# Optimization experiments

Measured on AMD Instinct MI355X. Metric: run time of the kernel, lower is better.

Reference implementation:

```python
import jax, jax.numpy as jnp
import numpy as np

B, C, D = 4096, 1000, 3072


def setup_inputs() -> dict:
    key = jax.random.key(0)
    k1, k2, k3, k4 = jax.random.split(key, 4)
    scale = 1.0
    return {
        "z": jax.random.normal(k1, (B, D), dtype=jnp.float32),
        "sldj": jax.random.normal(k2, (B,), dtype=jnp.float32),
        "labels": jax.random.randint(k3, (B,), 0, C),
        "beta": jnp.ones((), dtype=jnp.float32),
        "means": jax.random.normal(k4, (C, D), dtype=jnp.float32) * scale,
    }


def reference(z, sldj, labels, beta, means):
    # dists[i,j] = -0.5 * ||z_i - mu_j||^2, via a^2 + b^2 - 2ab GEMM trick
    z2 = jnp.sum(z * z, axis=1, keepdims=True)          # [B,1]
    m2 = jnp.sum(means * means, axis=1)[None, :]        # [1,C]
    cross = jnp.einsum('bd,cd->bc', z, means)           # [B,C] GEMM
    dists = -0.5 * (z2 + m2 - 2.0 * cross)              # [B,C]

    log_pz = jax.nn.logsumexp(dists, axis=1)            # [B]
    # cross_entropy(dists, labels) = mean(logsumexp - dists[i, y_i])
    picked = jnp.take_along_axis(dists, labels[:, None], axis=1)[:, 0]
    loss_cls = jnp.mean(log_pz - picked)
    loss_gen = -jnp.mean(log_pz + sldj) / z.shape[1]
    total = loss_gen + beta * loss_cls
    return total, loss_gen, loss_cls
```

## Files before the change

### kernel.cpp

```cpp
#include <hip/hip_runtime.h>
#include <hip/hip_bf16.h>
#include <cstdint>
#include <cstddef>

#define NB 4096
#define NC 1000
#define NCP 1024
#define ND 3072
#define NSL 4
#define KSL (ND / NSL)
#define BM 128
#define BN 128
#define BK 32
#define NT (KSL / BK)
#define ABUF (BM * BK)
#define BBUF (BN * BK)

typedef __attribute__((ext_vector_type(8))) __bf16 bf16x8;
typedef __attribute__((ext_vector_type(4))) float f32x4;
typedef __attribute__((ext_vector_type(4))) unsigned short u16x4;
typedef __attribute__((ext_vector_type(4))) _Float16 f16x4;
typedef unsigned short u16;

__device__ __forceinline__ u16 f2bf_rne(float x) {
    uint32_t u = __float_as_uint(x);
    uint32_t r = (u + 0x7fffu + ((u >> 16) & 1u)) >> 16;
    return (u16)r;
}

__global__ __launch_bounds__(256) void convert_all_kernel(
        const float* __restrict__ z, const float* __restrict__ means,
        u16* __restrict__ zb, u16* __restrict__ mb,
        float* __restrict__ z2, float* __restrict__ m2) {
    const int bidx = blockIdx.x;
    const int tid = threadIdx.x;
    const float* src;
    u16* dst;
    float* sq;
    bool pad = false;
    if (bidx < NB) {
        src = z + (size_t)bidx * ND;
        dst = zb + (size_t)bidx * ND;
        sq = z2 + bidx;
    } else {
        const int mr = bidx - NB;
        dst = mb + (size_t)mr * ND;
        sq = m2 + mr;
        src = means + (size_t)mr * ND;
        pad = (mr >= NC);
    }
    if (!pad) {
        const float4* s = (const float4*)src;
        float acc = 0.f;
#pragma unroll
        for (int i = 0; i < 3; ++i) {
            const int idx = tid + i * 256;
            float4 v = s[idx];
            acc = fmaf(v.x, v.x, acc);
            acc = fmaf(v.y, v.y, acc);
            acc = fmaf(v.z, v.z, acc);
            acc = fmaf(v.w, v.w, acc);
            u16x4 o;
            o.x = f2bf_rne(v.x); o.y = f2bf_rne(v.y);
            o.z = f2bf_rne(v.z); o.w = f2bf_rne(v.w);
            *(u16x4*)(dst + idx * 4) = o;
        }
#pragma unroll
        for (int off = 32; off > 0; off >>= 1) acc += __shfl_xor(acc, off, 64);
        __shared__ float ssum[4];
        const int wid = tid >> 6, lane = tid & 63;
        if (lane == 0) ssum[wid] = acc;
        __syncthreads();
        if (tid == 0) sq[0] = ssum[0] + ssum[1] + ssum[2] + ssum[3];
    } else {
        u16x4 z4 = (u16x4){0, 0, 0, 0};
#pragma unroll
        for (int i = 0; i < 3; ++i) *(u16x4*)(dst + (tid + i * 256) * 4) = z4;
        if (tid == 0) sq[0] = 1e30f;
    }
}

#define GLOAD_LDS16(gp, lp)                                            \
    __builtin_amdgcn_global_load_lds(                                  \
        (const __attribute__((address_space(1))) void*)(gp),           \
        (__attribute__((address_space(3))) void*)(lp), 16, 0, 0)

__global__ __launch_bounds__(256, 4) void gemm_kernel(
        const u16* __restrict__ zb, const u16* __restrict__ mb,
        _Float16* __restrict__ crossh) {
    __shared__ u16 As[2 * ABUF];
    __shared__ u16 Bs[2 * BBUF];

    const int tid  = threadIdx.x;
    const int wid  = tid >> 6;
    const int lane = tid & 63;
    const int wr   = wid >> 1;
    const int wc   = wid & 1;
    const int lrow = lane & 15;
    const int kgrp = lane >> 4;

    const int bid = blockIdx.x;
    const int w = (bid & 7) * 128 + (bid >> 3);
    const int bcol8 = w & 7;
    const int brow  = ((w >> 3) & 31) * BM;
    const int ksl   = w >> 8;
    const int bcol  = bcol8 * BN;
    const int kbase = ksl * KSL;

    f32x4 acc[4][4];
#pragma unroll
    for (int m = 0; m < 4; ++m)
#pragma unroll
        for (int n = 0; n < 4; ++n) acc[m][n] = (f32x4){0.f, 0.f, 0.f, 0.f};

    const u16* gA[2]; const u16* gB[2];
    u16* lA[2];       u16* lB[2];
#pragma unroll
    for (int g = 0; g < 2; ++g) {
        const int c = g * 256 + tid;
        const int r = c >> 2, p = c & 3, s = p ^ ((r >> 1) & 3);
        gA[g] = zb + (size_t)(brow + r) * ND + kbase + s * 8;
        gB[g] = mb + (size_t)(bcol + r) * ND + kbase + s * 8;
        lA[g] = As + (g * 256 + wid * 64) * 8;
        lB[g] = Bs + (g * 256 + wid * 64) * 8;
    }

#define STAGE(tt) do {                                                   \
        const int bb_ = (tt) & 1;                                        \
        const int ko_ = (tt) * BK;                                       \
        GLOAD_LDS16(gA[0] + ko_, lA[0] + bb_ * ABUF);                    \
        GLOAD_LDS16(gA[1] + ko_, lA[1] + bb_ * ABUF);                    \
        GLOAD_LDS16(gB[0] + ko_, lB[0] + bb_ * BBUF);                    \
        GLOAD_LDS16(gB[1] + ko_, lB[1] + bb_ * BBUF);                    \
    } while (0)

#define COMP(tt) do {                                                    \
        const int cb_ = (tt) & 1;                                        \
        const u16* Ac = As + cb_ * ABUF;                                 \
        const u16* Bc = Bs + cb_ * BBUF;                                 \
        const int pk = kgrp ^ ((lrow >> 1) & 3);                         \
        bf16x8 a0 = *(const bf16x8*)&Ac[(wr * 64 +  0 + lrow) * BK + pk * 8]; \
        bf16x8 a1 = *(const bf16x8*)&Ac[(wr * 64 + 16 + lrow) * BK + pk * 8]; \
        bf16x8 a2 = *(const bf16x8*)&Ac[(wr * 64 + 32 + lrow) * BK + pk * 8]; \
        bf16x8 a3 = *(const bf16x8*)&Ac[(wr * 64 + 48 + lrow) * BK + pk * 8]; \
        _Pragma("unroll")                                                \
        for (int n = 0; n < 4; ++n) {                                    \
            bf16x8 bn = *(const bf16x8*)&Bc[(wc * 64 + n * 16 + lrow) * BK + pk * 8]; \
            acc[0][n] = __builtin_amdgcn_mfma_f32_16x16x32_bf16(a0, bn, acc[0][n], 0, 0, 0); \
            acc[1][n] = __builtin_amdgcn_mfma_f32_16x16x32_bf16(a1, bn, acc[1][n], 0, 0, 0); \
            acc[2][n] = __builtin_amdgcn_mfma_f32_16x16x32_bf16(a2, bn, acc[2][n], 0, 0, 0); \
            acc[3][n] = __builtin_amdgcn_mfma_f32_16x16x32_bf16(a3, bn, acc[3][n], 0, 0, 0); \
        }                                                                \
    } while (0)

    STAGE(0);

    for (int t = 0; t < NT; ++t) {
        asm volatile("s_waitcnt vmcnt(0)" ::: "memory");
        __builtin_amdgcn_s_barrier();
        __builtin_amdgcn_sched_barrier(0);
        if (t + 1 < NT) STAGE(t + 1);
        __builtin_amdgcn_sched_barrier(0);
        COMP(t);
    }

#undef STAGE
#undef COMP

    _Float16* outp = crossh + (size_t)ksl * NB * NCP;
#pragma unroll
    for (int n = 0; n < 4; ++n) {
        const int gcol = bcol + wc * 64 + n * 16 + lrow;
#pragma unroll
        for (int m = 0; m < 4; ++m) {
#pragma unroll
            for (int r = 0; r < 4; ++r) {
                const int grow = brow + wr * 64 + m * 16 + kgrp * 4 + r;
                outp[(size_t)grow * NCP + gcol] = (_Float16)acc[m][n][r];
            }
        }
    }
}

__global__ __launch_bounds__(256) void row_lse_kernel(
        const _Float16* __restrict__ crossh, const float* __restrict__ m2,
        const int* __restrict__ labels, const float* __restrict__ sldj,
        float* __restrict__ outA, float* __restrict__ outB) {
    const int row = blockIdx.x;
    const int tid = threadIdx.x;

    float a0 = 0.f, a1 = 0.f, a2 = 0.f, a3 = 0.f;
#pragma unroll
    for (int s = 0; s < NSL; ++s) {
        f16x4 h = ((const f16x4*)(crossh + ((size_t)s * NB + row) * NCP))[tid];
        a0 += (float)h.x; a1 += (float)h.y; a2 += (float)h.z; a3 += (float)h.w;
    }
    float4 mm = ((const float4*)m2)[tid];
    float4 v;
    v.x = a0 - 0.5f * mm.x;
    v.y = a1 - 0.5f * mm.y;
    v.z = a2 - 0.5f * mm.z;
    v.w = a3 - 0.5f * mm.w;

    float mx = fmaxf(fmaxf(v.x, v.y), fmaxf(v.z, v.w));
#pragma unroll
    for (int off = 32; off > 0; off >>= 1) mx = fmaxf(mx, __shfl_xor(mx, off, 64));
    __shared__ float smax[4], ssum[4];
    const int wid = tid >> 6, lane = tid & 63;
    if (lane == 0) smax[wid] = mx;
    __syncthreads();
    const float bm = fmaxf(fmaxf(smax[0], smax[1]), fmaxf(smax[2], smax[3]));

    float s = expf(v.x - bm) + expf(v.y - bm) + expf(v.z - bm) + expf(v.w - bm);
#pragma unroll
    for (int off = 32; off > 0; off >>= 1) s += __shfl_xor(s, off, 64);
    if (lane == 0) ssum[wid] = s;
    __syncthreads();
    if (tid == 0) {
        const float tot = ssum[0] + ssum[1] + ssum[2] + ssum[3];
        const float lpz = bm + logf(tot);
        const int lab = labels[row];
        float pick = 0.f;
#pragma unroll
        for (int si = 0; si < NSL; ++si)
            pick += (float)crossh[((size_t)si * NB + row) * NCP + lab];
        pick -= 0.5f * m2[lab];
        outA[row] = lpz - pick;
        outB[row] = lpz + sldj[row];
    }
}

__global__ __launch_bounds__(1024) void finalize_kernel(
        const float* __restrict__ a, const float* __restrict__ b,
        const float* __restrict__ z2, const float* __restrict__ beta,
        float* __restrict__ out) {
    __shared__ float sa[1024], sb[1024], sz[1024];
    const int tid = threadIdx.x;
    float va = 0.f, vb = 0.f, vz = 0.f;
    for (int i = tid; i < NB; i += 1024) {
        va += a[i]; vb += b[i]; vz += z2[i];
    }
    sa[tid] = va; sb[tid] = vb; sz[tid] = vz;
    __syncthreads();
    for (int s = 512; s > 0; s >>= 1) {
        if (tid < s) {
            sa[tid] += sa[tid + s];
            sb[tid] += sb[tid + s];
            sz[tid] += sz[tid + s];
        }
        __syncthreads();
    }
    if (tid == 0) {
        const float loss_cls = sa[0] / (float)NB;
        const float mean_lpz_sldj = sb[0] / (float)NB - 0.5f * (sz[0] / (float)NB);
        const float loss_gen = -mean_lpz_sldj / (float)ND;
        const float total = loss_gen + beta[0] * loss_cls;
        out[0] = total;
        out[1] = loss_gen;
        out[2] = loss_cls;
    }
}

extern "C" void kernel_launch(void* const* d_in, const int* in_sizes, int n_in,
                              void* d_out, int out_size, void* d_ws, size_t ws_size,
                              hipStream_t stream) {
    const float* z      = (const float*)d_in[0];
    const float* sldj   = (const float*)d_in[1];
    const int*   labels = (const int*)d_in[2];
    const float* beta   = (const float*)d_in[3];
    const float* means  = (const float*)d_in[4];
    float* out = (float*)d_out;

    char* ws = (char*)d_ws;
    size_t off = 0;
    u16* zb = (u16*)(ws + off);           off += (size_t)NB * ND * 2;
    u16* mb = (u16*)(ws + off);           off += (size_t)NCP * ND * 2;
    float* z2 = (float*)(ws + off);       off += (size_t)NB * 4;
    float* m2 = (float*)(ws + off);       off += (size_t)NCP * 4;
    _Float16* crossh = (_Float16*)(ws + off); off += (size_t)NSL * NB * NCP * 2;
    float* ra = (float*)(ws + off);       off += (size_t)NB * 4;
    float* rb = (float*)(ws + off);       off += (size_t)NB * 4;

    convert_all_kernel<<<NB + NCP, 256, 0, stream>>>(z, means, zb, mb, z2, m2);
    gemm_kernel<<<8 * 32 * NSL, 256, 0, stream>>>(zb, mb, crossh);
    row_lse_kernel<<<NB, 256, 0, stream>>>(crossh, m2, labels, sldj, ra, rb);
    finalize_kernel<<<1, 1024, 0, stream>>>(ra, rb, z2, beta, out);
}
```

Measured before the change: 66.07 us.

## Enlarge GEMM block tile to 256x256 with 16 waves and 4-stage LDS pipeline

Each GEMM workgroup now covers a 256x256 output tile with 1024 threads, where each of 16 waves computes a 64x64 sub-tile. The grid shrinks to 256 blocks, roughly one per CU. The LDS ring grows to four buffers with three stages prefetched ahead, and waits use partial vmcnt so loads overlap more compute. The aim is better global-memory reuse per block and more latency hiding. In exchange, launch_bounds(1024,4) caps per-wave registers tightly, which risks spilling the 64-float accumulator, and LDS use rises to 128KB per block.

```diff
diff --git a/kernel.cpp b/kernel.cpp
--- a/kernel.cpp
+++ b/kernel.cpp
@@ -9,8 +9,8 @@
 #define ND 3072
 #define NSL 4
 #define KSL (ND / NSL)
-#define BM 128
-#define BN 128
+#define BM 256
+#define BN 256
 #define BK 32
 #define NT (KSL / BK)
 #define ABUF (BM * BK)
@@ -85,26 +85,26 @@
         (const __attribute__((address_space(1))) void*)(gp),           \
         (__attribute__((address_space(3))) void*)(lp), 16, 0, 0)
 
-__global__ __launch_bounds__(256, 4) void gemm_kernel(
+__global__ __launch_bounds__(1024, 4) void gemm_kernel(
         const u16* __restrict__ zb, const u16* __restrict__ mb,
         _Float16* __restrict__ crossh) {
-    __shared__ u16 As[2 * ABUF];
-    __shared__ u16 Bs[2 * BBUF];
+    __shared__ u16 As[4 * ABUF];
+    __shared__ u16 Bs[4 * BBUF];
 
     const int tid  = threadIdx.x;
     const int wid  = tid >> 6;
     const int lane = tid & 63;
-    const int wr   = wid >> 1;
-    const int wc   = wid & 1;
+    const int wrr  = (wid >> 2) * 64;
+    const int wcc  = (wid & 3) * 64;
     const int lrow = lane & 15;
     const int kgrp = lane >> 4;
 
     const int bid = blockIdx.x;
-    const int w = (bid & 7) * 128 + (bid >> 3);
-    const int bcol8 = w & 7;
-    const int brow  = ((w >> 3) & 31) * BM;
-    const int ksl   = w >> 8;
-    const int bcol  = bcol8 * BN;
+    const int w = (bid & 7) * 32 + (bid >> 3);
+    const int ksl  = w >> 6;
+    const int rem  = w & 63;
+    const int brow = (rem >> 2) * BM;
+    const int bcol = (rem & 3) * BN;
     const int kbase = ksl * KSL;
 
     f32x4 acc[4][4];
@@ -113,39 +113,37 @@
 #pragma unroll
         for (int n = 0; n < 4; ++n) acc[m][n] = (f32x4){0.f, 0.f, 0.f, 0.f};
 
-    const u16* gA[2]; const u16* gB[2];
-    u16* lA[2];       u16* lB[2];
-#pragma unroll
-    for (int g = 0; g < 2; ++g) {
-        const int c = g * 256 + tid;
-        const int r = c >> 2, p = c & 3, s = p ^ ((r >> 1) & 3);
-        gA[g] = zb + (size_t)(brow + r) * ND + kbase + s * 8;
-        gB[g] = mb + (size_t)(bcol + r) * ND + kbase + s * 8;
-        lA[g] = As + (g * 256 + wid * 64) * 8;
-        lB[g] = Bs + (g * 256 + wid * 64) * 8;
+    const u16* gA;
+    const u16* gB;
+    u16* lA;
+    u16* lB;
+    {
+        const int r = tid >> 2, p = tid & 3, s = p ^ ((r >> 1) & 3);
+        gA = zb + (size_t)(brow + r) * ND + kbase + s * 8;
+        gB = mb + (size_t)(bcol + r) * ND + kbase + s * 8;
+        lA = As + wid * 512;
+        lB = Bs + wid * 512;
     }
 
 #define STAGE(tt) do {                                                   \
-        const int bb_ = (tt) & 1;                                        \
+        const int bb_ = (tt) & 3;                                        \
         const int ko_ = (tt) * BK;                                       \
-        GLOAD_LDS16(gA[0] + ko_, lA[0] + bb_ * ABUF);                    \
-        GLOAD_LDS16(gA[1] + ko_, lA[1] + bb_ * ABUF);                    \
-        GLOAD_LDS16(gB[0] + ko_, lB[0] + bb_ * BBUF);                    \
-        GLOAD_LDS16(gB[1] + ko_, lB[1] + bb_ * BBUF);                    \
+        GLOAD_LDS16(gA + ko_, lA + bb_ * ABUF);                          \
+        GLOAD_LDS16(gB + ko_, lB + bb_ * BBUF);                          \
     } while (0)
 
 #define COMP(tt) do {                                                    \
-        const int cb_ = (tt) & 1;                                        \
+        const int cb_ = (tt) & 3;                                        \
         const u16* Ac = As + cb_ * ABUF;                                 \
         const u16* Bc = Bs + cb_ * BBUF;                                 \
         const int pk = kgrp ^ ((lrow >> 1) & 3);                         \
-        bf16x8 a0 = *(const bf16x8*)&Ac[(wr * 64 +  0 + lrow) * BK + pk * 8]; \
-        bf16x8 a1 = *(const bf16x8*)&Ac[(wr * 64 + 16 + lrow) * BK + pk * 8]; \
-        bf16x8 a2 = *(const bf16x8*)&Ac[(wr * 64 + 32 + lrow) * BK + pk * 8]; \
-        bf16x8 a3 = *(const bf16x8*)&Ac[(wr * 64 + 48 + lrow) * BK + pk * 8]; \
+        bf16x8 a0 = *(const bf16x8*)&Ac[(wrr +  0 + lrow) * BK + pk * 8]; \
+        bf16x8 a1 = *(const bf16x8*)&Ac[(wrr + 16 + lrow) * BK + pk * 8]; \
+        bf16x8 a2 = *(const bf16x8*)&Ac[(wrr + 32 + lrow) * BK + pk * 8]; \
+        bf16x8 a3 = *(const bf16x8*)&Ac[(wrr + 48 + lrow) * BK + pk * 8]; \
         _Pragma("unroll")                                                \
         for (int n = 0; n < 4; ++n) {                                    \
-            bf16x8 bn = *(const bf16x8*)&Bc[(wc * 64 + n * 16 + lrow) * BK + pk * 8]; \
+            bf16x8 bn = *(const bf16x8*)&Bc[(wcc + n * 16 + lrow) * BK + pk * 8]; \
             acc[0][n] = __builtin_amdgcn_mfma_f32_16x16x32_bf16(a0, bn, acc[0][n], 0, 0, 0); \
             acc[1][n] = __builtin_amdgcn_mfma_f32_16x16x32_bf16(a1, bn, acc[1][n], 0, 0, 0); \
             acc[2][n] = __builtin_amdgcn_mfma_f32_16x16x32_bf16(a2, bn, acc[2][n], 0, 0, 0); \
@@ -153,16 +151,24 @@
         }                                                                \
     } while (0)
 
-    STAGE(0);
-
-    for (int t = 0; t < NT; ++t) {
-        asm volatile("s_waitcnt vmcnt(0)" ::: "memory");
+    STAGE(0); STAGE(1); STAGE(2);
+
+    for (int t = 0; t < NT - 2; ++t) {
+        asm volatile("s_waitcnt vmcnt(4)" ::: "memory");
         __builtin_amdgcn_s_barrier();
         __builtin_amdgcn_sched_barrier(0);
-        if (t + 1 < NT) STAGE(t + 1);
+        if (t + 3 < NT) STAGE(t + 3);
         __builtin_amdgcn_sched_barrier(0);
         COMP(t);
     }
+    asm volatile("s_waitcnt vmcnt(2)" ::: "memory");
+    __builtin_amdgcn_s_barrier();
+    __builtin_amdgcn_sched_barrier(0);
+    COMP(NT - 2);
+    asm volatile("s_waitcnt vmcnt(0)" ::: "memory");
+    __builtin_amdgcn_s_barrier();
+    __builtin_amdgcn_sched_barrier(0);
+    COMP(NT - 1);
 
 #undef STAGE
 #undef COMP
@@ -170,12 +176,12 @@
     _Float16* outp = crossh + (size_t)ksl * NB * NCP;
 #pragma unroll
     for (int n = 0; n < 4; ++n) {
-        const int gcol = bcol + wc * 64 + n * 16 + lrow;
+        const int gcol = bcol + wcc + n * 16 + lrow;
 #pragma unroll
         for (int m = 0; m < 4; ++m) {
 #pragma unroll
             for (int r = 0; r < 4; ++r) {
-                const int grow = brow + wr * 64 + m * 16 + kgrp * 4 + r;
+                const int grow = brow + wrr + m * 16 + kgrp * 4 + r;
                 outp[(size_t)grow * NCP + gcol] = (_Float16)acc[m][n][r];
             }
         }
@@ -282,7 +288,7 @@
     float* rb = (float*)(ws + off);       off += (size_t)NB * 4;
 
     convert_all_kernel<<<NB + NCP, 256, 0, stream>>>(z, means, zb, mb, z2, m2);
-    gemm_kernel<<<8 * 32 * NSL, 256, 0, stream>>>(zb, mb, crossh);
+    gemm_kernel<<<8 * 32 * NSL / 4, 1024, 0, stream>>>(zb, mb, crossh);
     row_lse_kernel<<<NB, 256, 0, stream>>>(crossh, m2, labels, sldj, ra, rb);
     finalize_kernel<<<1, 1024, 0, stream>>>(ra, rb, z2, beta, out);
 }
```

Result: faster. 60.44 us, median of 3 (-8.5%).
